# Optimization experiments

Measured on AMD Instinct MI355X. Metric: run time of the kernel, lower is better.

The kernel has to match this reference:

```python
import jax, jax.numpy as jnp
import numpy as np


def gcn_conv(x, src, dst, W, b, num_nodes):
    """PyG GCNConv: out = D^{-1/2} (A+I) D^{-1/2} X W + b (self-loops already in src/dst)."""
    h = x @ W  # [N, F_out]
    ones = jnp.ones(dst.shape[0], dtype=x.dtype)
    deg = jax.ops.segment_sum(ones, dst, num_segments=num_nodes)  # in-degree incl self-loop
    dis = jnp.where(deg > 0, jax.lax.rsqrt(deg), jnp.zeros_like(deg))  # deg^{-1/2}
    norm = dis[src] * dis[dst]  # [E]
    msg = h[src] * norm[:, None]  # gather + scale, [E, F_out]
    out = jax.ops.segment_sum(msg, dst, num_segments=num_nodes) + b
    return out


def setup_inputs() -> dict:
    key = jax.random.key(0)
    k = jax.random.split(key, 6)
    N, E, F_IN, HID, C = 100000, 3200000, 128, 16, 8
    x = jax.random.normal(k[0], (N, F_IN), dtype=jnp.float32)
    edge_index = jax.random.randint(k[1], (2, E), 0, N, dtype=jnp.int64)
    W1 = jax.random.normal(k[2], (F_IN, HID), dtype=jnp.float32) * (1.0 / np.sqrt(F_IN))
    b1 = jnp.zeros((HID,), dtype=jnp.float32)
    W2 = jax.random.normal(k[3], (HID, C), dtype=jnp.float32) * (1.0 / np.sqrt(HID))
    b2 = jnp.zeros((C,), dtype=jnp.float32)
    return {"x": x, "edge_index": edge_index, "W1": W1, "b1": b1, "W2": W2, "b2": b2}


def reference(x, edge_index, W1, b1, W2, b2):
    N = x.shape[0]
    loop = jnp.arange(N, dtype=edge_index.dtype)
    src = jnp.concatenate([edge_index[0], loop])  # add self-loops
    dst = jnp.concatenate([edge_index[1], loop])
    h = gcn_conv(x, src, dst, W1, b1, N)
    h = jax.nn.relu(h)  # dropout is identity in eval mode
    out = gcn_conv(h, src, dst, W2, b2, N)
    return out
```

## Files before the change

kernel.cpp:

```cpp
#include <hip/hip_runtime.h>
#include <hip/hip_fp16.h>

#define F_IN 128
#define HID 16
#define C_OUT 8
#define BSH 6
#define BSZ 64
#define G1 1024
#define NBMAX 1600
#define CAP 3072

typedef unsigned int uint;

__device__ inline int chunk_of_block(int blk) {
    return ((blk & 7) << 7) | (blk >> 3);
}

__global__ void count_kernel(const int* __restrict__ dst, uint* __restrict__ counts,
                             int E, int CE, int NB) {
    __shared__ uint h[NBMAX];
    int chunk = chunk_of_block(blockIdx.x), tid = threadIdx.x;
    for (int i = tid; i < NB; i += 256) h[i] = 0;
    __syncthreads();
    int base = chunk * CE, end = min(E, base + CE);
    int n = end - base;
    if (n > 0) {
        int n4 = n >> 2;
        const int4* p = reinterpret_cast<const int4*>(dst + base);
        for (int i = tid; i < n4; i += 256) {
            int4 d = p[i];
            atomicAdd(&h[((uint)d.x) >> BSH], 1u);
            atomicAdd(&h[((uint)d.y) >> BSH], 1u);
            atomicAdd(&h[((uint)d.z) >> BSH], 1u);
            atomicAdd(&h[((uint)d.w) >> BSH], 1u);
        }
        for (int i = base + (n4 << 2) + tid; i < end; i += 256)
            atomicAdd(&h[((uint)dst[i]) >> BSH], 1u);
    }
    __syncthreads();
    for (int i = tid; i < NB; i += 256)
        counts[(size_t)i * G1 + chunk] = h[i];
}

__global__ void scanA_kernel(uint* __restrict__ counts, uint* __restrict__ btot) {
    int b = blockIdx.x, tid = threadIdx.x;
    int lane = tid & 63, wid = tid >> 6;
    uint v = counts[(size_t)b * G1 + tid];
    uint inc = v;
#pragma unroll
    for (int o = 1; o < 64; o <<= 1) {
        uint t = __shfl_up(inc, o);
        if (lane >= o) inc += t;
    }
    __shared__ uint wsum[16];
    if (lane == 63) wsum[wid] = inc;
    __syncthreads();
    if (tid < 16) {
        uint w = wsum[tid], iw = w;
#pragma unroll
        for (int o = 1; o < 16; o <<= 1) {
            uint t = __shfl_up(iw, o);
            if (tid >= o) iw += t;
        }
        wsum[tid] = iw - w;
        if (tid == 15) btot[b] = iw;
    }
    __syncthreads();
    counts[(size_t)b * G1 + tid] = wsum[wid] + inc - v;
}

__global__ void scanB_kernel(const uint* __restrict__ btot, uint* __restrict__ bbase,
                             int NB, int E) {
    __shared__ uint wsum[4];
    __shared__ uint ctot;
    int tid = threadIdx.x, lane = tid & 63, wid = tid >> 6;
    uint base = 0;
    for (int c0 = 0; c0 < NB; c0 += 256) {
        int i = c0 + tid;
        uint v = (i < NB) ? btot[i] : 0u;
        uint inc = v;
#pragma unroll
        for (int o = 1; o < 64; o <<= 1) {
            uint t = __shfl_up(inc, o);
            if (lane >= o) inc += t;
        }
        if (lane == 63) wsum[wid] = inc;
        __syncthreads();
        if (tid == 0) {
            uint s = 0;
#pragma unroll
            for (int k = 0; k < 4; ++k) { uint t = wsum[k]; wsum[k] = s; s += t; }
            ctot = s;
        }
        __syncthreads();
        if (i < NB) bbase[i] = base + wsum[wid] + inc - v;
        base += ctot;
        __syncthreads();
    }
    if (tid == 0) bbase[NB] = (uint)E;
}

__global__ void place_kernel(const int* __restrict__ src, const int* __restrict__ dst,
                             const uint* __restrict__ offs, const uint* __restrict__ bbase,
                             uint* __restrict__ rec, int E, int CE, int NB) {
    __shared__ uint cur[NBMAX];
    int chunk = chunk_of_block(blockIdx.x), tid = threadIdx.x;
    for (int i = tid; i < NB; i += 256)
        cur[i] = bbase[i] + offs[(size_t)i * G1 + chunk];
    __syncthreads();
    int base = chunk * CE, end = min(E, base + CE);
    int n = end - base;
    if (n <= 0) return;
    int n4 = n >> 2;
    const int4* ps = reinterpret_cast<const int4*>(src + base);
    const int4* pd = reinterpret_cast<const int4*>(dst + base);
    for (int i = tid; i < n4; i += 256) {
        int4 s = ps[i];
        int4 d = pd[i];
        uint p0 = atomicAdd(&cur[((uint)d.x) >> BSH], 1u);
        rec[p0] = (uint)s.x | (((uint)d.x & (BSZ - 1)) << 17);
        uint p1 = atomicAdd(&cur[((uint)d.y) >> BSH], 1u);
        rec[p1] = (uint)s.y | (((uint)d.y & (BSZ - 1)) << 17);
        uint p2 = atomicAdd(&cur[((uint)d.z) >> BSH], 1u);
        rec[p2] = (uint)s.z | (((uint)d.z & (BSZ - 1)) << 17);
        uint p3 = atomicAdd(&cur[((uint)d.w) >> BSH], 1u);
        rec[p3] = (uint)s.w | (((uint)d.w & (BSZ - 1)) << 17);
    }
    for (int i = base + (n4 << 2) + tid; i < end; i += 256) {
        int d = dst[i];
        uint b = ((uint)d) >> BSH;
        uint p = atomicAdd(&cur[b], 1u);
        rec[p] = (uint)src[i] | (((uint)d & (BSZ - 1)) << 17);
    }
}

__global__ void sortdis_kernel(uint* __restrict__ rec, const uint* __restrict__ bbase,
                               uint* __restrict__ nstart, float* __restrict__ dis,
                               int N, int NB) {
    __shared__ uint tmp[CAP];
    __shared__ uint h[BSZ];
    __shared__ uint cur[BSZ];
    int b = blockIdx.x, tid = threadIdx.x;
    uint lane = (uint)(tid & 63);
    if (tid < BSZ) h[tid] = 0;
    uint s0 = bbase[b], s1 = bbase[b + 1];
    uint seg = min(s1 - s0, (uint)CAP);
    __syncthreads();

    uint hreg = 0;
    uint i = (uint)tid;
    uint wbase = (uint)(tid & ~63);
    while (wbase + 64 <= seg) {
        uint r = rec[s0 + i];
        tmp[i] = r;
        uint bin = (r >> 17) & 63u;
        unsigned long long bal[6];
#pragma unroll
        for (int bit = 0; bit < 6; ++bit)
            bal[bit] = __ballot((bin >> bit) & 1u);
        unsigned long long m = ~0ull;
#pragma unroll
        for (int bit = 0; bit < 6; ++bit)
            m &= ((lane >> bit) & 1u) ? bal[bit] : ~bal[bit];
        hreg += (uint)__popcll(m);
        i += 256; wbase += 256;
    }
    while (i < seg) {
        uint r = rec[s0 + i];
        tmp[i] = r;
        atomicAdd(&h[(r >> 17) & 63u], 1u);
        i += 256;
    }
    if (hreg) atomicAdd(&h[lane], hreg);
    __syncthreads();

    if (tid < BSZ) {
        uint v = h[tid], inc = v;
#pragma unroll
        for (int o = 1; o < BSZ; o <<= 1) {
            uint t = __shfl_up(inc, o);
            if (tid >= o) inc += t;
        }
        uint excl = inc - v;
        cur[tid] = s0 + excl;
        int n = b * BSZ + tid;
        if (n < N) {
            nstart[n] = s0 + excl;
            dis[n] = rsqrtf((float)v + 1.0f);
        }
    }
    if (b == NB - 1 && tid == 0) nstart[N] = s1;
    __syncthreads();

    i = (uint)tid;
    wbase = (uint)(tid & ~63);
    while (wbase + 64 <= seg) {
        uint r = tmp[i];
        uint bin = (r >> 17) & 63u;
        unsigned long long m = ~0ull;
#pragma unroll
        for (int bit = 0; bit < 6; ++bit) {
            unsigned long long bal = __ballot((bin >> bit) & 1u);
            m &= ((bin >> bit) & 1u) ? bal : ~bal;
        }
        uint leader = (uint)__ffsll((unsigned long long)m) - 1u;
        uint rank = (uint)__popcll(m & ((1ull << lane) - 1ull));
        uint basep = 0;
        if (lane == leader) basep = atomicAdd(&cur[bin], (uint)__popcll(m));
        basep = (uint)__shfl((int)basep, (int)leader);
        rec[basep + rank] = r & 0x1FFFFu;
        i += 256; wbase += 256;
    }
    while (i < seg) {
        uint r = tmp[i];
        uint p = atomicAdd(&cur[(r >> 17) & 63u], 1u);
        rec[p] = r & 0x1FFFFu;
        i += 256;
    }
}

__global__ void h1_kernel(const float* __restrict__ x, const float* __restrict__ W1,
                          const float* __restrict__ dis, __half* __restrict__ hs1, int N) {
    __shared__ float w[F_IN * HID];
    for (int t = threadIdx.x; t < F_IN * HID; t += blockDim.x) w[t] = W1[t];
    __syncthreads();
    int row = blockIdx.x * blockDim.x + threadIdx.x;
    if (row >= N) return;
    float acc[HID];
#pragma unroll
    for (int j = 0; j < HID; ++j) acc[j] = 0.f;
    const float4* xr = reinterpret_cast<const float4*>(x + (size_t)row * F_IN);
#pragma unroll 4
    for (int k4 = 0; k4 < F_IN / 4; ++k4) {
        float4 v = xr[k4];
        int k = k4 * 4;
#pragma unroll
        for (int j = 0; j < HID; ++j) {
            acc[j] += v.x * w[(k + 0) * HID + j] + v.y * w[(k + 1) * HID + j]
                    + v.z * w[(k + 2) * HID + j] + v.w * w[(k + 3) * HID + j];
        }
    }
    float d = dis[row];
    uint u[8];
#pragma unroll
    for (int p = 0; p < 8; ++p) {
        __half2 hh = __floats2half2_rn(acc[2 * p] * d, acc[2 * p + 1] * d);
        u[p] = *reinterpret_cast<uint*>(&hh);
    }
    uint4* o = reinterpret_cast<uint4*>(hs1 + ((size_t)row << 4));
    o[0] = make_uint4(u[0], u[1], u[2], u[3]);
    o[1] = make_uint4(u[4], u[5], u[6], u[7]);
}

__device__ inline void acc8(uint4 v, float* a) {
    float2 f;
    f = __half22float2(*reinterpret_cast<const __half2*>(&v.x)); a[0] += f.x; a[1] += f.y;
    f = __half22float2(*reinterpret_cast<const __half2*>(&v.y)); a[2] += f.x; a[3] += f.y;
    f = __half22float2(*reinterpret_cast<const __half2*>(&v.z)); a[4] += f.x; a[5] += f.y;
    f = __half22float2(*reinterpret_cast<const __half2*>(&v.w)); a[6] += f.x; a[7] += f.y;
}

__global__ void agg1_kernel(const uint* __restrict__ rec, const uint* __restrict__ nstart,
                            const __half* __restrict__ hs1, const float* __restrict__ dis,
                            const float* __restrict__ b1v, const float* __restrict__ W2,
                            float* __restrict__ hs2, int N) {
    __shared__ float w2s[HID * C_OUT];
    __shared__ float b1s[HID];
    int tid = threadIdx.x;
    if (tid < HID * C_OUT) w2s[tid] = W2[tid];
    if (tid < HID) b1s[tid] = b1v[tid];
    __syncthreads();
    int ldn = tid >> 2;
    uint q  = (uint)(tid & 1);
    uint rr = (uint)((tid >> 1) & 1);
    int n = blockIdx.x * 64 + ldn;
    if (n >= N) return;
    uint e = nstart[n], en = nstart[n + 1];
    const uint4* hb = reinterpret_cast<const uint4*>(hs1) + q;
    float a[8];
#pragma unroll
    for (int j = 0; j < 8; ++j) a[j] = 0.f;
    uint i = e + rr;
    while (i + 14 < en) {
        uint i0 = __builtin_nontemporal_load(rec + i);
        uint i1 = __builtin_nontemporal_load(rec + i + 2);
        uint i2 = __builtin_nontemporal_load(rec + i + 4);
        uint i3 = __builtin_nontemporal_load(rec + i + 6);
        uint i4 = __builtin_nontemporal_load(rec + i + 8);
        uint i5 = __builtin_nontemporal_load(rec + i + 10);
        uint i6 = __builtin_nontemporal_load(rec + i + 12);
        uint i7 = __builtin_nontemporal_load(rec + i + 14);
        uint4 v0 = hb[(size_t)i0 << 1];
        uint4 v1 = hb[(size_t)i1 << 1];
        uint4 v2 = hb[(size_t)i2 << 1];
        uint4 v3 = hb[(size_t)i3 << 1];
        uint4 v4 = hb[(size_t)i4 << 1];
        uint4 v5 = hb[(size_t)i5 << 1];
        uint4 v6 = hb[(size_t)i6 << 1];
        uint4 v7 = hb[(size_t)i7 << 1];
        acc8(v0, a); acc8(v1, a); acc8(v2, a); acc8(v3, a);
        acc8(v4, a); acc8(v5, a); acc8(v6, a); acc8(v7, a);
        i += 16;
    }
    while (i < en) {
        uint i0 = __builtin_nontemporal_load(rec + i);
        uint4 v = hb[(size_t)i0 << 1];
        acc8(v, a);
        i += 2;
    }
#pragma unroll
    for (int j = 0; j < 8; ++j) a[j] += __shfl_xor(a[j], 2);
    uint4 sv = hb[(size_t)n << 1];
    float s[8];
    {
        float2 f;
        f = __half22float2(*reinterpret_cast<const __half2*>(&sv.x)); s[0] = f.x; s[1] = f.y;
        f = __half22float2(*reinterpret_cast<const __half2*>(&sv.y)); s[2] = f.x; s[3] = f.y;
        f = __half22float2(*reinterpret_cast<const __half2*>(&sv.z)); s[4] = f.x; s[5] = f.y;
        f = __half22float2(*reinterpret_cast<const __half2*>(&sv.w)); s[6] = f.x; s[7] = f.y;
    }
    float dv = dis[n];
    float r[8];
#pragma unroll
    for (int j = 0; j < 8; ++j)
        r[j] = fmaxf(dv * (a[j] + s[j]) + b1s[q * 8 + j], 0.f);
    float p[C_OUT];
#pragma unroll
    for (int c = 0; c < C_OUT; ++c) {
        float t = 0.f;
#pragma unroll
        for (int j = 0; j < 8; ++j) t += r[j] * w2s[(q * 8 + j) * C_OUT + c];
        p[c] = t;
    }
#pragma unroll
    for (int c = 0; c < C_OUT; ++c) p[c] += __shfl_xor(p[c], 1);
    if (rr == 0) {
        float4 o;
        o.x = p[q * 4 + 0] * dv;
        o.y = p[q * 4 + 1] * dv;
        o.z = p[q * 4 + 2] * dv;
        o.w = p[q * 4 + 3] * dv;
        *reinterpret_cast<float4*>(hs2 + ((size_t)n << 3) + (q << 2)) = o;
    }
}

__global__ void agg2_kernel(const uint* __restrict__ rec, const uint* __restrict__ nstart,
                            const float* __restrict__ hs2, const float* __restrict__ dis,
                            const float* __restrict__ b2v, float* __restrict__ out, int N) {
    int tid = threadIdx.x;
    int ldn = tid >> 2;
    uint q  = (uint)(tid & 1);
    uint rr = (uint)((tid >> 1) & 1);
    int n = blockIdx.x * 64 + ldn;
    if (n >= N) return;
    uint e = nstart[n], en = nstart[n + 1];
    const float* hq = hs2 + (q << 2);
    float ax = 0.f, ay = 0.f, az = 0.f, aw = 0.f;
    uint i = e + rr;
    while (i + 14 < en) {
        uint i0 = __builtin_nontemporal_load(rec + i);
        uint i1 = __builtin_nontemporal_load(rec + i + 2);
        uint i2 = __builtin_nontemporal_load(rec + i + 4);
        uint i3 = __builtin_nontemporal_load(rec + i + 6);
        uint i4 = __builtin_nontemporal_load(rec + i + 8);
        uint i5 = __builtin_nontemporal_load(rec + i + 10);
        uint i6 = __builtin_nontemporal_load(rec + i + 12);
        uint i7 = __builtin_nontemporal_load(rec + i + 14);
        float4 v0 = *reinterpret_cast<const float4*>(hq + ((size_t)i0 << 3));
        float4 v1 = *reinterpret_cast<const float4*>(hq + ((size_t)i1 << 3));
        float4 v2 = *reinterpret_cast<const float4*>(hq + ((size_t)i2 << 3));
        float4 v3 = *reinterpret_cast<const float4*>(hq + ((size_t)i3 << 3));
        float4 v4 = *reinterpret_cast<const float4*>(hq + ((size_t)i4 << 3));
        float4 v5 = *reinterpret_cast<const float4*>(hq + ((size_t)i5 << 3));
        float4 v6 = *reinterpret_cast<const float4*>(hq + ((size_t)i6 << 3));
        float4 v7 = *reinterpret_cast<const float4*>(hq + ((size_t)i7 << 3));
        ax += ((v0.x + v1.x) + (v2.x + v3.x)) + ((v4.x + v5.x) + (v6.x + v7.x));
        ay += ((v0.y + v1.y) + (v2.y + v3.y)) + ((v4.y + v5.y) + (v6.y + v7.y));
        az += ((v0.z + v1.z) + (v2.z + v3.z)) + ((v4.z + v5.z) + (v6.z + v7.z));
        aw += ((v0.w + v1.w) + (v2.w + v3.w)) + ((v4.w + v5.w) + (v6.w + v7.w));
        i += 16;
    }
    while (i < en) {
        uint i0 = __builtin_nontemporal_load(rec + i);
        float4 v = *reinterpret_cast<const float4*>(hq + ((size_t)i0 << 3));
        ax += v.x; ay += v.y; az += v.z; aw += v.w;
        i += 2;
    }
    ax += __shfl_xor(ax, 2);
    ay += __shfl_xor(ay, 2);
    az += __shfl_xor(az, 2);
    aw += __shfl_xor(aw, 2);
    if (rr == 0) {
        float4 self = *reinterpret_cast<const float4*>(hq + ((size_t)n << 3));
        float dv = dis[n];
        float4 o;
        o.x = dv * (ax + self.x) + b2v[q * 4 + 0];
        o.y = dv * (ay + self.y) + b2v[q * 4 + 1];
        o.z = dv * (az + self.z) + b2v[q * 4 + 2];
        o.w = dv * (aw + self.w) + b2v[q * 4 + 3];
        *reinterpret_cast<float4*>(out + ((size_t)n << 3) + (q << 2)) = o;
    }
}

extern "C" void kernel_launch(void* const* d_in, const int* in_sizes, int n_in,
                              void* d_out, int out_size, void* d_ws, size_t ws_size,
                              hipStream_t stream) {
    const float* x  = (const float*)d_in[0];
    const int*   ei = (const int*)d_in[1];
    const float* W1 = (const float*)d_in[2];
    const float* b1 = (const float*)d_in[3];
    const float* W2 = (const float*)d_in[4];
    const float* b2 = (const float*)d_in[5];
    float* out = (float*)d_out;

    int N = in_sizes[0] / F_IN;
    int E = in_sizes[1] / 2;
    const int* src = ei;
    const int* dst = ei + E;

    int NB = (N + BSZ - 1) / BSZ;
    int CE = (((E + G1 - 1) / G1) + 3) & ~3;

    float*  hs2   = (float*)d_ws;
    __half* hs1   = (__half*)(hs2 + (size_t)8 * N);
    float*  dis   = (float*)(hs2 + (size_t)16 * N);
    uint*   nstart = (uint*)(dis + N);
    uint*   rec   = nstart + N + 1;
    uint*   counts = rec + E;
    uint*   btot  = counts + (size_t)NB * G1;
    uint*   bbase = btot + NB;

    const int B = 256;
    count_kernel<<<G1, B, 0, stream>>>(dst, counts, E, CE, NB);
    scanA_kernel<<<NB, G1, 0, stream>>>(counts, btot);
    scanB_kernel<<<1, B, 0, stream>>>(btot, bbase, NB, E);
    place_kernel<<<G1, B, 0, stream>>>(src, dst, counts, bbase, rec, E, CE, NB);
    sortdis_kernel<<<NB, B, 0, stream>>>(rec, bbase, nstart, dis, N, NB);
    h1_kernel<<<(N + B - 1) / B, B, 0, stream>>>(x, W1, dis, hs1, N);
    agg1_kernel<<<(N + 63) / 64, B, 0, stream>>>(rec, nstart, hs1, dis, b1, W2, hs2, N);
    agg2_kernel<<<(N + 63) / 64, B, 0, stream>>>(rec, nstart, hs2, dis, b2, out, N);
}
```

Measured before the change: 165.8 us.

## Use two threads per node with 16-byte vector edge-index loads in aggregation

Both aggregation kernels now give each node 2 threads instead of 4, which removes the edge-parity split and its cross-lane reduction. Each thread loads neighbor indices as aligned 4-wide vectors after a scalar alignment prologue, and the rec array base is padded to a 16-byte boundary so those loads are legal. The goal is fewer index-load instructions and fewer idle lanes for low-degree nodes. In exchange each thread walks a longer serial chain of gathers, which lowers the number of loads in flight per node.

```diff
diff --git a/kernel.cpp b/kernel.cpp
--- a/kernel.cpp
+++ b/kernel.cpp
@@ -11,6 +11,7 @@
 #define CAP 3072
 
 typedef unsigned int uint;
+typedef uint ui4 __attribute__((ext_vector_type(4)));
 
 __device__ inline int chunk_of_block(int blk) {
     return ((blk & 7) << 7) | (blk >> 3);
@@ -270,46 +271,48 @@
     if (tid < HID * C_OUT) w2s[tid] = W2[tid];
     if (tid < HID) b1s[tid] = b1v[tid];
     __syncthreads();
-    int ldn = tid >> 2;
-    uint q  = (uint)(tid & 1);
-    uint rr = (uint)((tid >> 1) & 1);
-    int n = blockIdx.x * 64 + ldn;
+    int ldn = tid >> 1, q = tid & 1;
+    int n = blockIdx.x * 128 + ldn;
     if (n >= N) return;
     uint e = nstart[n], en = nstart[n + 1];
     const uint4* hb = reinterpret_cast<const uint4*>(hs1) + q;
     float a[8];
 #pragma unroll
     for (int j = 0; j < 8; ++j) a[j] = 0.f;
-    uint i = e + rr;
-    while (i + 14 < en) {
-        uint i0 = __builtin_nontemporal_load(rec + i);
-        uint i1 = __builtin_nontemporal_load(rec + i + 2);
-        uint i2 = __builtin_nontemporal_load(rec + i + 4);
-        uint i3 = __builtin_nontemporal_load(rec + i + 6);
-        uint i4 = __builtin_nontemporal_load(rec + i + 8);
-        uint i5 = __builtin_nontemporal_load(rec + i + 10);
-        uint i6 = __builtin_nontemporal_load(rec + i + 12);
-        uint i7 = __builtin_nontemporal_load(rec + i + 14);
-        uint4 v0 = hb[(size_t)i0 << 1];
-        uint4 v1 = hb[(size_t)i1 << 1];
-        uint4 v2 = hb[(size_t)i2 << 1];
-        uint4 v3 = hb[(size_t)i3 << 1];
-        uint4 v4 = hb[(size_t)i4 << 1];
-        uint4 v5 = hb[(size_t)i5 << 1];
-        uint4 v6 = hb[(size_t)i6 << 1];
-        uint4 v7 = hb[(size_t)i7 << 1];
+    while (e < en && (e & 3u)) {
+        uint4 v = hb[(size_t)rec[e] << 1];
+        acc8(v, a);
+        ++e;
+    }
+    while (e + 8 <= en) {
+        ui4 rA = __builtin_nontemporal_load(reinterpret_cast<const ui4*>(rec + e));
+        ui4 rB = __builtin_nontemporal_load(reinterpret_cast<const ui4*>(rec + e + 4));
+        uint4 v0 = hb[(size_t)rA.x << 1];
+        uint4 v1 = hb[(size_t)rA.y << 1];
+        uint4 v2 = hb[(size_t)rA.z << 1];
+        uint4 v3 = hb[(size_t)rA.w << 1];
+        uint4 v4 = hb[(size_t)rB.x << 1];
+        uint4 v5 = hb[(size_t)rB.y << 1];
+        uint4 v6 = hb[(size_t)rB.z << 1];
+        uint4 v7 = hb[(size_t)rB.w << 1];
         acc8(v0, a); acc8(v1, a); acc8(v2, a); acc8(v3, a);
         acc8(v4, a); acc8(v5, a); acc8(v6, a); acc8(v7, a);
-        i += 16;
-    }
-    while (i < en) {
-        uint i0 = __builtin_nontemporal_load(rec + i);
-        uint4 v = hb[(size_t)i0 << 1];
+        e += 8;
+    }
+    if (e + 4 <= en) {
+        ui4 rA = __builtin_nontemporal_load(reinterpret_cast<const ui4*>(rec + e));
+        uint4 v0 = hb[(size_t)rA.x << 1];
+        uint4 v1 = hb[(size_t)rA.y << 1];
+        uint4 v2 = hb[(size_t)rA.z << 1];
+        uint4 v3 = hb[(size_t)rA.w << 1];
+        acc8(v0, a); acc8(v1, a); acc8(v2, a); acc8(v3, a);
+        e += 4;
+    }
+    while (e < en) {
+        uint4 v = hb[(size_t)rec[e] << 1];
         acc8(v, a);
-        i += 2;
-    }
-#pragma unroll
-    for (int j = 0; j < 8; ++j) a[j] += __shfl_xor(a[j], 2);
+        ++e;
+    }
     uint4 sv = hb[(size_t)n << 1];
     float s[8];
     {
@@ -334,72 +337,71 @@
     }
 #pragma unroll
     for (int c = 0; c < C_OUT; ++c) p[c] += __shfl_xor(p[c], 1);
-    if (rr == 0) {
-        float4 o;
-        o.x = p[q * 4 + 0] * dv;
-        o.y = p[q * 4 + 1] * dv;
-        o.z = p[q * 4 + 2] * dv;
-        o.w = p[q * 4 + 3] * dv;
-        *reinterpret_cast<float4*>(hs2 + ((size_t)n << 3) + (q << 2)) = o;
-    }
+    float4 o;
+    o.x = p[q * 4 + 0] * dv;
+    o.y = p[q * 4 + 1] * dv;
+    o.z = p[q * 4 + 2] * dv;
+    o.w = p[q * 4 + 3] * dv;
+    *reinterpret_cast<float4*>(hs2 + ((size_t)n << 3) + (q << 2)) = o;
 }
 
 __global__ void agg2_kernel(const uint* __restrict__ rec, const uint* __restrict__ nstart,
                             const float* __restrict__ hs2, const float* __restrict__ dis,
                             const float* __restrict__ b2v, float* __restrict__ out, int N) {
     int tid = threadIdx.x;
-    int ldn = tid >> 2;
-    uint q  = (uint)(tid & 1);
-    uint rr = (uint)((tid >> 1) & 1);
-    int n = blockIdx.x * 64 + ldn;
+    int ldn = tid >> 1, q = tid & 1;
+    int n = blockIdx.x * 128 + ldn;
     if (n >= N) return;
     uint e = nstart[n], en = nstart[n + 1];
     const float* hq = hs2 + (q << 2);
     float ax = 0.f, ay = 0.f, az = 0.f, aw = 0.f;
-    uint i = e + rr;
-    while (i + 14 < en) {
-        uint i0 = __builtin_nontemporal_load(rec + i);
-        uint i1 = __builtin_nontemporal_load(rec + i + 2);
-        uint i2 = __builtin_nontemporal_load(rec + i + 4);
-        uint i3 = __builtin_nontemporal_load(rec + i + 6);
-        uint i4 = __builtin_nontemporal_load(rec + i + 8);
-        uint i5 = __builtin_nontemporal_load(rec + i + 10);
-        uint i6 = __builtin_nontemporal_load(rec + i + 12);
-        uint i7 = __builtin_nontemporal_load(rec + i + 14);
-        float4 v0 = *reinterpret_cast<const float4*>(hq + ((size_t)i0 << 3));
-        float4 v1 = *reinterpret_cast<const float4*>(hq + ((size_t)i1 << 3));
-        float4 v2 = *reinterpret_cast<const float4*>(hq + ((size_t)i2 << 3));
-        float4 v3 = *reinterpret_cast<const float4*>(hq + ((size_t)i3 << 3));
-        float4 v4 = *reinterpret_cast<const float4*>(hq + ((size_t)i4 << 3));
-        float4 v5 = *reinterpret_cast<const float4*>(hq + ((size_t)i5 << 3));
-        float4 v6 = *reinterpret_cast<const float4*>(hq + ((size_t)i6 << 3));
-        float4 v7 = *reinterpret_cast<const float4*>(hq + ((size_t)i7 << 3));
+    while (e < en && (e & 3u)) {
+        float4 v = *reinterpret_cast<const float4*>(hq + ((size_t)rec[e] << 3));
+        ax += v.x; ay += v.y; az += v.z; aw += v.w;
+        ++e;
+    }
+    while (e + 8 <= en) {
+        ui4 rA = __builtin_nontemporal_load(reinterpret_cast<const ui4*>(rec + e));
+        ui4 rB = __builtin_nontemporal_load(reinterpret_cast<const ui4*>(rec + e + 4));
+        float4 v0 = *reinterpret_cast<const float4*>(hq + ((size_t)rA.x << 3));
+        float4 v1 = *reinterpret_cast<const float4*>(hq + ((size_t)rA.y << 3));
+        float4 v2 = *reinterpret_cast<const float4*>(hq + ((size_t)rA.z << 3));
+        float4 v3 = *reinterpret_cast<const float4*>(hq + ((size_t)rA.w << 3));
+        float4 v4 = *reinterpret_cast<const float4*>(hq + ((size_t)rB.x << 3));
+        float4 v5 = *reinterpret_cast<const float4*>(hq + ((size_t)rB.y << 3));
+        float4 v6 = *reinterpret_cast<const float4*>(hq + ((size_t)rB.z << 3));
+        float4 v7 = *reinterpret_cast<const float4*>(hq + ((size_t)rB.w << 3));
         ax += ((v0.x + v1.x) + (v2.x + v3.x)) + ((v4.x + v5.x) + (v6.x + v7.x));
         ay += ((v0.y + v1.y) + (v2.y + v3.y)) + ((v4.y + v5.y) + (v6.y + v7.y));
         az += ((v0.z + v1.z) + (v2.z + v3.z)) + ((v4.z + v5.z) + (v6.z + v7.z));
         aw += ((v0.w + v1.w) + (v2.w + v3.w)) + ((v4.w + v5.w) + (v6.w + v7.w));
-        i += 16;
-    }
-    while (i < en) {
-        uint i0 = __builtin_nontemporal_load(rec + i);
-        float4 v = *reinterpret_cast<const float4*>(hq + ((size_t)i0 << 3));
+        e += 8;
+    }
+    if (e + 4 <= en) {
+        ui4 rA = __builtin_nontemporal_load(reinterpret_cast<const ui4*>(rec + e));
+        float4 v0 = *reinterpret_cast<const float4*>(hq + ((size_t)rA.x << 3));
+        float4 v1 = *reinterpret_cast<const float4*>(hq + ((size_t)rA.y << 3));
+        float4 v2 = *reinterpret_cast<const float4*>(hq + ((size_t)rA.z << 3));
+        float4 v3 = *reinterpret_cast<const float4*>(hq + ((size_t)rA.w << 3));
+        ax += (v0.x + v1.x) + (v2.x + v3.x);
+        ay += (v0.y + v1.y) + (v2.y + v3.y);
+        az += (v0.z + v1.z) + (v2.z + v3.z);
+        aw += (v0.w + v1.w) + (v2.w + v3.w);
+        e += 4;
+    }
+    while (e < en) {
+        float4 v = *reinterpret_cast<const float4*>(hq + ((size_t)rec[e] << 3));
         ax += v.x; ay += v.y; az += v.z; aw += v.w;
-        i += 2;
-    }
-    ax += __shfl_xor(ax, 2);
-    ay += __shfl_xor(ay, 2);
-    az += __shfl_xor(az, 2);
-    aw += __shfl_xor(aw, 2);
-    if (rr == 0) {
-        float4 self = *reinterpret_cast<const float4*>(hq + ((size_t)n << 3));
-        float dv = dis[n];
-        float4 o;
-        o.x = dv * (ax + self.x) + b2v[q * 4 + 0];
-        o.y = dv * (ay + self.y) + b2v[q * 4 + 1];
-        o.z = dv * (az + self.z) + b2v[q * 4 + 2];
-        o.w = dv * (aw + self.w) + b2v[q * 4 + 3];
-        *reinterpret_cast<float4*>(out + ((size_t)n << 3) + (q << 2)) = o;
-    }
+        ++e;
+    }
+    float4 self = *reinterpret_cast<const float4*>(hq + ((size_t)n << 3));
+    float dv = dis[n];
+    float4 o;
+    o.x = dv * (ax + self.x) + b2v[q * 4 + 0];
+    o.y = dv * (ay + self.y) + b2v[q * 4 + 1];
+    o.z = dv * (az + self.z) + b2v[q * 4 + 2];
+    o.w = dv * (aw + self.w) + b2v[q * 4 + 3];
+    *reinterpret_cast<float4*>(out + ((size_t)n << 3) + (q << 2)) = o;
 }
 
 extern "C" void kernel_launch(void* const* d_in, const int* in_sizes, int n_in,
@@ -421,14 +423,14 @@
     int NB = (N + BSZ - 1) / BSZ;
     int CE = (((E + G1 - 1) / G1) + 3) & ~3;
 
-    float*  hs2   = (float*)d_ws;
-    __half* hs1   = (__half*)(hs2 + (size_t)8 * N);
-    float*  dis   = (float*)(hs2 + (size_t)16 * N);
+    float*  hs2    = (float*)d_ws;
+    __half* hs1    = (__half*)(hs2 + (size_t)8 * N);
+    float*  dis    = (float*)(hs2 + (size_t)16 * N);
     uint*   nstart = (uint*)(dis + N);
-    uint*   rec   = nstart + N + 1;
+    uint*   rec    = nstart + ((N + 1 + 3) & ~3);
     uint*   counts = rec + E;
-    uint*   btot  = counts + (size_t)NB * G1;
-    uint*   bbase = btot + NB;
+    uint*   btot   = counts + (size_t)NB * G1;
+    uint*   bbase  = btot + NB;
 
     const int B = 256;
     count_kernel<<<G1, B, 0, stream>>>(dst, counts, E, CE, NB);
@@ -437,6 +439,6 @@
     place_kernel<<<G1, B, 0, stream>>>(src, dst, counts, bbase, rec, E, CE, NB);
     sortdis_kernel<<<NB, B, 0, stream>>>(rec, bbase, nstart, dis, N, NB);
     h1_kernel<<<(N + B - 1) / B, B, 0, stream>>>(x, W1, dis, hs1, N);
-    agg1_kernel<<<(N + 63) / 64, B, 0, stream>>>(rec, nstart, hs1, dis, b1, W2, hs2, N);
-    agg2_kernel<<<(N + 63) / 64, B, 0, stream>>>(rec, nstart, hs2, dis, b2, out, N);
-}
+    agg1_kernel<<<(N + 127) / 128, B, 0, stream>>>(rec, nstart, hs1, dis, b1, W2, hs2, N);
+    agg2_kernel<<<(N + 127) / 128, B, 0, stream>>>(rec, nstart, hs2, dis, b2, out, N);
+}
```

Result: faster. 160.3 us (-3.3%).
